# Optimization experiments

Hardware: AMD Instinct MI355X
Metric: run time of the kernel (lower is better)

## Reference

```python
import jax, jax.numpy as jnp
import numpy as np
from jax import lax

B, S, E, SD = 8, 4096, 1024, 8


def setup_inputs() -> dict:
    key = jax.random.key(0)
    ks = jax.random.split(key, 4)
    x = jax.random.normal(ks[0], (B, S, E), dtype=jnp.float32)
    W_in = jax.random.normal(ks[1], (E, E + SD), dtype=jnp.float32) / np.sqrt(E)
    b_in = jnp.zeros((E + SD,), dtype=jnp.float32)
    W_g = jax.random.normal(ks[2], (E + SD, SD), dtype=jnp.float32) / np.sqrt(E + SD)
    b_g = jnp.zeros((SD,), dtype=jnp.float32)
    W_out = jax.random.normal(ks[3], (E + SD, E), dtype=jnp.float32) / np.sqrt(E + SD)
    b_out = jnp.zeros((E,), dtype=jnp.float32)
    return {"x": x, "W_in": W_in, "b_in": b_in, "W_g": W_g, "b_g": b_g,
            "W_out": W_out, "b_out": b_out}


def reference(x, W_in, b_in, W_g, b_g, W_out, b_out):
    embed_dim = W_in.shape[0]
    # State-independent projections batched over the whole sequence.
    combined = jnp.einsum('bse,ec->bsc', x, W_in) + b_in            # [B,S,E+SD]
    embed = combined[..., :embed_dim]                                # [B,S,E]
    state_in = combined[..., embed_dim:]                             # [B,S,SD]
    gate = jax.nn.sigmoid(jnp.einsum('bsc,cd->bsd', combined, W_g) + b_g)  # [B,S,SD]

    # Only the tiny gated state recurrence is sequential.
    def step(state, gs):
        g, si = gs
        new = g * state + (1.0 - g) * si
        return new, new

    state0 = jnp.zeros((x.shape[0], state_in.shape[-1]), dtype=x.dtype)
    g_t = jnp.moveaxis(gate, 1, 0)        # [S,B,SD]
    si_t = jnp.moveaxis(state_in, 1, 0)   # [S,B,SD]
    final_state, states = lax.scan(step, state0, (g_t, si_t))
    states = jnp.moveaxis(states, 0, 1)   # [B,S,SD]

    out = jnp.einsum('bsc,cd->bsd', jnp.concatenate([embed, states], axis=-1), W_out) + b_out
    return out, final_state
```

## Files before the change

### kernel.cpp

```cpp
#include <hip/hip_runtime.h>

typedef unsigned short ushort_t;
typedef __attribute__((ext_vector_type(8))) short short8;
typedef __attribute__((ext_vector_type(4))) float floatx4;

#define B_ 8
#define S_ 4096
#define E_ 1024
#define SD_ 8
#define M_TOTAL (B_ * S_)
#define NC 1032
#define NCH 256
#define CHS (S_ / NCH)

__device__ __forceinline__ ushort_t f2bf(float f) {
    union { float f; unsigned u; } v; v.f = f;
    unsigned u = v.u;
    unsigned r = (u + 0x7fffu + ((u >> 16) & 1u)) >> 16;
    return (ushort_t)r;
}
__device__ __forceinline__ float bf2f(ushort_t h) {
    union { unsigned u; float f; } v; v.u = ((unsigned)h) << 16;
    return v.f;
}

__device__ __forceinline__ void stage16(ushort_t* lds_base_uniform, const ushort_t* g) {
    __builtin_amdgcn_global_load_lds(
        (const __attribute__((address_space(1))) void*)g,
        (__attribute__((address_space(3))) void*)lds_base_uniform, 16, 0, 0);
}


__global__ void wcomb_kernel(const float* __restrict__ W_in, const float* __restrict__ Wg,
                             float* __restrict__ Wc) {
    const int k = blockIdx.x;
    const int lane = threadIdx.x;
    float acc[8] = {0.f,0.f,0.f,0.f,0.f,0.f,0.f,0.f};
    for (int c = lane; c < NC; c += 64) {
        float w = W_in[(size_t)k * NC + c];
#pragma unroll
        for (int d = 0; d < 8; d++) acc[d] += w * Wg[(size_t)c * 8 + d];
    }
#pragma unroll
    for (int d = 0; d < 8; d++) {
#pragma unroll
        for (int off = 32; off >= 1; off >>= 1) acc[d] += __shfl_xor(acc[d], off);
    }
    if (lane == 0) {
#pragma unroll
        for (int d = 0; d < 8; d++) Wc[k * 8 + d] = acc[d];
    }
}

__global__ void prep_winb(const float* __restrict__ W, ushort_t* __restrict__ O) {
    int i = blockIdx.x * 256 + threadIdx.x;
    int k = i >> 8, j0 = (i & 255) * 4;
    float4 v = *(const float4*)(W + (size_t)k * NC + j0);
    ushort4 o;
    o.x = f2bf(v.x); o.y = f2bf(v.y); o.z = f2bf(v.z); o.w = f2bf(v.w);
    *(ushort4*)(O + (size_t)k * E_ + j0) = o;
}

__global__ void prep_wouts(const float* __restrict__ W, ushort_t* __restrict__ O) {
    int idx = blockIdx.x * 256 + threadIdx.x;
    int n = idx >> 10, j = idx & 1023;
    O[idx] = f2bf(W[(size_t)j * E_ + n]);
}

__global__ void prep_small(const float* __restrict__ W_in, const float* __restrict__ Wc,
                           const float* __restrict__ W_out, const float* __restrict__ b_in,
                           const float* __restrict__ Wg, const float* __restrict__ bg,
                           ushort_t* __restrict__ BT16, ushort_t* __restrict__ WoutT2,
                           float* __restrict__ bias16) {
    int idx = blockIdx.x * 256 + threadIdx.x;
    if (idx < 32768) {
        int n = idx >> 10, k = idx & 1023;
        float v;
        if (n < 8)        v = W_in[(size_t)k * NC + 1024 + n];
        else if (n < 16)  v = Wc[k * 8 + (n - 8)];
        else              v = 0.f;
        BT16[idx] = f2bf(v);
    } else {
        int i2 = idx - 32768;
        int n = i2 >> 5, k2 = i2 & 31;
        float v = (k2 < 8) ? W_out[(size_t)(1024 + k2) * E_ + n] : 0.f;
        WoutT2[i2] = f2bf(v);
    }
    if (idx < 32) {
        float s;
        if (idx < 8) s = b_in[1024 + idx];
        else if (idx < 16) {
            int d = idx - 8;
            s = bg[d];
            for (int j = 0; j < NC; j++) s += b_in[j] * Wg[(size_t)j * 8 + d];
        } else s = 0.f;
        bias16[idx] = s;
    }
}

__global__ void bias2_kernel(const float* __restrict__ b_in, const float* __restrict__ W_out,
                             const float* __restrict__ b_out, float* __restrict__ bias2) {
    int n = blockIdx.x * 64 + threadIdx.x;
    float acc = b_out[n];
    for (int j = 0; j < E_; j++) acc += b_in[j] * W_out[(size_t)j * E_ + n];
    bias2[n] = acc;
}

template <bool OUT_BF16, bool EXTRA>
__global__ __launch_bounds__(256, 2) void gemm_bt(
    const ushort_t* __restrict__ A, const ushort_t* __restrict__ BT,
    const ushort_t* __restrict__ A2, const ushort_t* __restrict__ BT2,
    void* __restrict__ Cout, const float* __restrict__ bias,
    int K, int lda, int ldb, int lda2, int ldb2, int ldc)
{
    __shared__ __align__(16) ushort_t sA[128 * 32];
    __shared__ __align__(16) ushort_t sB[128 * 32];
    const int tid = threadIdx.x;
    const int wave = tid >> 6;
    const int lane = tid & 63;

    const int gx = gridDim.x;
    int flat = blockIdx.y * gx + blockIdx.x;
    const int band_size = 8 * gx;
    int band = flat / band_size;
    int r = flat - band * band_size;
    const int m0 = (band * 8 + (r & 7)) * 128;
    const int n0 = (r >> 3) * 128;

    const int wm = wave >> 1, wn = wave & 1;
    const int fr = lane & 15, fq = lane >> 4;
    const int sr = lane >> 2;
    const int sc = (lane & 3) * 8;

    floatx4 acc[4][4];
#pragma unroll
    for (int i = 0; i < 4; i++)
#pragma unroll
        for (int j = 0; j < 4; j++) acc[i][j] = (floatx4)0.f;

    const ushort_t* gA = A + (size_t)(m0 + wave * 32 + sr) * lda + sc;
    const ushort_t* gB = BT + (size_t)(n0 + wave * 32 + sr) * ldb + sc;

    for (int k0 = 0; k0 < K; k0 += 32) {
        __syncthreads();
        stage16(&sA[(wave * 32 + 0) * 32], gA + k0);
        stage16(&sA[(wave * 32 + 16) * 32], gA + (size_t)16 * lda + k0);
        stage16(&sB[(wave * 32 + 0) * 32], gB + k0);
        stage16(&sB[(wave * 32 + 16) * 32], gB + (size_t)16 * ldb + k0);
        __syncthreads();

        short8 a[4], b[4];
#pragma unroll
        for (int i = 0; i < 4; i++)
            a[i] = *(const short8*)&sA[(wm * 64 + i * 16 + fr) * 32 + fq * 8];
#pragma unroll
        for (int j = 0; j < 4; j++)
            b[j] = *(const short8*)&sB[(wn * 64 + j * 16 + fr) * 32 + fq * 8];
#pragma unroll
        for (int i = 0; i < 4; i++)
#pragma unroll
            for (int j = 0; j < 4; j++)
                acc[i][j] = __builtin_amdgcn_mfma_f32_16x16x32_bf16(a[i], b[j], acc[i][j], 0, 0, 0);
    }

    if constexpr (EXTRA) {
        const ushort_t* gA2 = A2 + (size_t)(m0 + wave * 32 + sr) * lda2 + sc;
        const ushort_t* gB2 = BT2 + (size_t)(n0 + wave * 32 + sr) * ldb2 + sc;
        __syncthreads();
        stage16(&sA[(wave * 32 + 0) * 32], gA2);
        stage16(&sA[(wave * 32 + 16) * 32], gA2 + (size_t)16 * lda2);
        stage16(&sB[(wave * 32 + 0) * 32], gB2);
        stage16(&sB[(wave * 32 + 16) * 32], gB2 + (size_t)16 * ldb2);
        __syncthreads();

        short8 a[4], b[4];
#pragma unroll
        for (int i = 0; i < 4; i++)
            a[i] = *(const short8*)&sA[(wm * 64 + i * 16 + fr) * 32 + fq * 8];
#pragma unroll
        for (int j = 0; j < 4; j++)
            b[j] = *(const short8*)&sB[(wn * 64 + j * 16 + fr) * 32 + fq * 8];
#pragma unroll
        for (int i = 0; i < 4; i++)
#pragma unroll
            for (int j = 0; j < 4; j++)
                acc[i][j] = __builtin_amdgcn_mfma_f32_16x16x32_bf16(a[i], b[j], acc[i][j], 0, 0, 0);
    }

#pragma unroll
    for (int i = 0; i < 4; i++) {
        int row = m0 + wm * 64 + i * 16 + fq * 4;
#pragma unroll
        for (int j = 0; j < 4; j++) {
            int col = n0 + wn * 64 + j * 16 + fr;
            float bv = bias ? bias[col] : 0.f;
#pragma unroll
            for (int r2 = 0; r2 < 4; r2++) {
                float v = acc[i][j][r2] + bv;
                if (OUT_BF16)
                    ((ushort_t*)Cout)[(size_t)(row + r2) * ldc + col] = f2bf(v);
                else
                    ((float*)Cout)[(size_t)(row + r2) * ldc + col] = v;
            }
        }
    }
}

__global__ __launch_bounds__(256) void skinny16_cvt(
    const float* __restrict__ X,
    const ushort_t* __restrict__ BT,
    const float* __restrict__ bias,
    ushort_t* __restrict__ xb,
    ushort_t* __restrict__ C)
{
    const int tid = threadIdx.x, wave = tid >> 6, lane = tid & 63;
    const int m0 = blockIdx.x * 64 + wave * 16;
    const int fr = lane & 15, fq = lane >> 4;
    floatx4 acc0 = (floatx4)0.f;
    const float*    px  = X  + (size_t)(m0 + fr) * E_ + fq * 8;
    ushort_t*       pxb = xb + (size_t)(m0 + fr) * E_ + fq * 8;
    const ushort_t* pb0 = BT + (size_t)fr * E_ + fq * 8;
    for (int k0 = 0; k0 < E_; k0 += 32) {
        float4 v0 = *(const float4*)(px + k0);
        float4 v1 = *(const float4*)(px + k0 + 4);
        short8 a;
        a[0] = (short)f2bf(v0.x); a[1] = (short)f2bf(v0.y);
        a[2] = (short)f2bf(v0.z); a[3] = (short)f2bf(v0.w);
        a[4] = (short)f2bf(v1.x); a[5] = (short)f2bf(v1.y);
        a[6] = (short)f2bf(v1.z); a[7] = (short)f2bf(v1.w);
        *(short8*)(pxb + k0) = a;
        short8 b0 = *(const short8*)(pb0 + k0);
        acc0 = __builtin_amdgcn_mfma_f32_16x16x32_bf16(a, b0, acc0, 0, 0, 0);
    }
#pragma unroll
    for (int r = 0; r < 4; r++) {
        int row = m0 + fq * 4 + r;
        C[(size_t)row * 32 + fr]      = f2bf(acc0[r] + bias[fr]);
        C[(size_t)row * 32 + 16 + fr] = (ushort_t)0;
    }
}

__global__ void scan_chunks(const ushort_t* __restrict__ comb,
                            float* __restrict__ chA, float* __restrict__ chB)
{
    const int c = blockIdx.x, lane = threadIdx.x;
    const int b = lane >> 3, d = lane & 7;
    float A = 1.f, Bv = 0.f;
    const int s0 = c * CHS;
    for (int s = s0; s < s0 + CHS; s++) {
        size_t m = (size_t)b * S_ + s;
        float z = bf2f(comb[m * 32 + 8 + d]);
        float g = 1.f / (1.f + __expf(-z));
        float si = bf2f(comb[m * 32 + d]);
        Bv = g * Bv + (1.f - g) * si;
        A *= g;
    }
    chA[c * 64 + lane] = A;
    chB[c * 64 + lane] = Bv;
}

__global__ void scan_apply(ushort_t* __restrict__ comb,
                           const float* __restrict__ chA, const float* __restrict__ chB,
                           float* __restrict__ final_state)
{
    const int c = blockIdx.x, lane = threadIdx.x;
    const int b = lane >> 3, d = lane & 7;
    float state = 0.f;
    for (int j = 0; j < c; j++)
        state = chA[j * 64 + lane] * state + chB[j * 64 + lane];
    const int s0 = c * CHS;
    for (int s = s0; s < s0 + CHS; s++) {
        size_t m = (size_t)b * S_ + s;
        float z = bf2f(comb[m * 32 + 8 + d]);
        float g = 1.f / (1.f + __expf(-z));
        float si = bf2f(comb[m * 32 + d]);
        state = g * state + (1.f - g) * si;
        comb[m * 32 + d] = f2bf(state);
    }
    if (c == NCH - 1) final_state[lane] = state;
}

extern "C" void kernel_launch(void* const* d_in, const int* in_sizes, int n_in,
                              void* d_out, int out_size, void* d_ws, size_t ws_size,
                              hipStream_t stream)
{
    (void)in_sizes; (void)n_in; (void)out_size; (void)ws_size;
    const float* x     = (const float*)d_in[0];
    const float* W_in  = (const float*)d_in[1];
    const float* b_in  = (const float*)d_in[2];
    const float* W_g   = (const float*)d_in[3];
    const float* b_g   = (const float*)d_in[4];
    const float* W_out = (const float*)d_in[5];
    const float* b_out = (const float*)d_in[6];

    ushort_t* xb     = (ushort_t*)d_ws;
    ushort_t* comb16 = xb + (size_t)M_TOTAL * E_;
    ushort_t* WbigT  = comb16 + (size_t)M_TOTAL * 32;
    ushort_t* Winb   = WbigT + (size_t)E_ * E_;
    ushort_t* WoutTa = Winb + (size_t)E_ * E_;
    ushort_t* WoutT2 = WoutTa + (size_t)E_ * E_;
    ushort_t* BT16   = WoutT2 + (size_t)E_ * 32;
    float*    Wc     = (float*)(BT16 + (size_t)32 * E_);
    float*    bias16 = Wc + 1024 * 8;
    float*    bias2v = bias16 + 32;
    float*    chA    = bias2v + E_;
    float*    chB    = chA + NCH * 64;

    float* outp = (float*)d_out;
    float* fs = outp + (size_t)M_TOTAL * E_;

    wcomb_kernel<<<E_, 64, 0, stream>>>(W_in, W_g, Wc);
    prep_winb<<<1024, 256, 0, stream>>>(W_in, Winb);
    prep_wouts<<<(E_ * E_) / 256, 256, 0, stream>>>(W_out, WoutTa);
    prep_small<<<256, 256, 0, stream>>>(W_in, Wc, W_out, b_in, W_g, b_g, BT16, WoutT2, bias16);
    bias2_kernel<<<E_ / 64, 64, 0, stream>>>(b_in, W_out, b_out, bias2v);

    gemm_bt<true, false><<<dim3(E_ / 128, E_ / 128), 256, 0, stream>>>(
        WoutTa, Winb, nullptr, nullptr, WbigT, nullptr, E_, E_, E_, 0, 0, E_);

    skinny16_cvt<<<M_TOTAL / 64, 256, 0, stream>>>(x, BT16, bias16, xb, comb16);

    scan_chunks<<<NCH, 64, 0, stream>>>(comb16, chA, chB);
    scan_apply<<<NCH, 64, 0, stream>>>(comb16, chA, chB, fs);

    gemm_bt<false, true><<<dim3(E_ / 128, M_TOTAL / 128), 256, 0, stream>>>(
        xb, WbigT, comb16, WoutT2, outp, bias2v, E_, E_, E_, 32, 32, E_);
}
```

Baseline: 502.6 us.

## Split skinny GEMM K across waves and fuse chunked scan into one block-scan kernel

The skinny x·W16 projection now gives each wave a quarter of K for a 16-row tile and reduces the partial sums in shared memory, so the grid has four times as many blocks. The two-kernel chunked scan, which recombined chunk prefixes serially, is replaced by one kernel per (batch, state-dim) pair. Each block computes 256 sub-chunk summaries, does a Hillis-Steele prefix scan in LDS, then applies the result. This removes one launch and the serial prefix loop, at the cost of more syncs and strided 2-byte global accesses.

```diff
diff --git a/kernel.cpp b/kernel.cpp
--- a/kernel.cpp
+++ b/kernel.cpp
@@ -10,8 +10,6 @@
 #define SD_ 8
 #define M_TOTAL (B_ * S_)
 #define NC 1032
-#define NCH 256
-#define CHS (S_ / NCH)
 
 __device__ __forceinline__ ushort_t f2bf(float f) {
     union { float f; unsigned u; } v; v.f = f;
@@ -214,70 +212,84 @@
     ushort_t* __restrict__ C)
 {
     const int tid = threadIdx.x, wave = tid >> 6, lane = tid & 63;
-    const int m0 = blockIdx.x * 64 + wave * 16;
+    const int m0 = blockIdx.x * 16;
     const int fr = lane & 15, fq = lane >> 4;
-    floatx4 acc0 = (floatx4)0.f;
-    const float*    px  = X  + (size_t)(m0 + fr) * E_ + fq * 8;
-    ushort_t*       pxb = xb + (size_t)(m0 + fr) * E_ + fq * 8;
-    const ushort_t* pb0 = BT + (size_t)fr * E_ + fq * 8;
-    for (int k0 = 0; k0 < E_; k0 += 32) {
-        float4 v0 = *(const float4*)(px + k0);
-        float4 v1 = *(const float4*)(px + k0 + 4);
+    const int k0w = wave * 256;
+
+    floatx4 acc = (floatx4)0.f;
+    const float*    px  = X  + (size_t)(m0 + fr) * E_ + k0w + fq * 8;
+    ushort_t*       pxb = xb + (size_t)(m0 + fr) * E_ + k0w + fq * 8;
+    const ushort_t* pb  = BT + (size_t)fr * E_ + k0w + fq * 8;
+#pragma unroll
+    for (int kk = 0; kk < 256; kk += 32) {
+        float4 v0 = *(const float4*)(px + kk);
+        float4 v1 = *(const float4*)(px + kk + 4);
         short8 a;
         a[0] = (short)f2bf(v0.x); a[1] = (short)f2bf(v0.y);
         a[2] = (short)f2bf(v0.z); a[3] = (short)f2bf(v0.w);
         a[4] = (short)f2bf(v1.x); a[5] = (short)f2bf(v1.y);
         a[6] = (short)f2bf(v1.z); a[7] = (short)f2bf(v1.w);
-        *(short8*)(pxb + k0) = a;
-        short8 b0 = *(const short8*)(pb0 + k0);
-        acc0 = __builtin_amdgcn_mfma_f32_16x16x32_bf16(a, b0, acc0, 0, 0, 0);
-    }
-#pragma unroll
-    for (int r = 0; r < 4; r++) {
-        int row = m0 + fq * 4 + r;
-        C[(size_t)row * 32 + fr]      = f2bf(acc0[r] + bias[fr]);
-        C[(size_t)row * 32 + 16 + fr] = (ushort_t)0;
-    }
-}
-
-__global__ void scan_chunks(const ushort_t* __restrict__ comb,
-                            float* __restrict__ chA, float* __restrict__ chB)
+        *(short8*)(pxb + kk) = a;
+        short8 b0 = *(const short8*)(pb + kk);
+        acc = __builtin_amdgcn_mfma_f32_16x16x32_bf16(a, b0, acc, 0, 0, 0);
+    }
+
+    __shared__ float red[4][16][16];
+#pragma unroll
+    for (int r = 0; r < 4; r++) red[wave][fq * 4 + r][fr] = acc[r];
+    __syncthreads();
+    const int row = tid >> 4, col = tid & 15;
+    float v = red[0][row][col] + red[1][row][col] + red[2][row][col] + red[3][row][col]
+            + bias[col];
+    C[(size_t)(m0 + row) * 32 + col]      = f2bf(v);
+    C[(size_t)(m0 + row) * 32 + 16 + col] = (ushort_t)0;
+}
+
+__global__ __launch_bounds__(256) void scan_fused(
+    ushort_t* __restrict__ comb, float* __restrict__ final_state)
 {
-    const int c = blockIdx.x, lane = threadIdx.x;
-    const int b = lane >> 3, d = lane & 7;
+    const int b = blockIdx.x >> 3, d = blockIdx.x & 7;
+    const int t = threadIdx.x;
+    __shared__ float sA[256], sB[256];
+    const size_t base = (size_t)b * S_ * 32;
+    const int s0 = t * 16;
+
     float A = 1.f, Bv = 0.f;
-    const int s0 = c * CHS;
-    for (int s = s0; s < s0 + CHS; s++) {
-        size_t m = (size_t)b * S_ + s;
-        float z = bf2f(comb[m * 32 + 8 + d]);
+    for (int s = s0; s < s0 + 16; s++) {
+        size_t m = base + (size_t)s * 32;
+        float z = bf2f(comb[m + 8 + d]);
         float g = 1.f / (1.f + __expf(-z));
-        float si = bf2f(comb[m * 32 + d]);
+        float si = bf2f(comb[m + d]);
         Bv = g * Bv + (1.f - g) * si;
         A *= g;
     }
-    chA[c * 64 + lane] = A;
-    chB[c * 64 + lane] = Bv;
-}
-
-__global__ void scan_apply(ushort_t* __restrict__ comb,
-                           const float* __restrict__ chA, const float* __restrict__ chB,
-                           float* __restrict__ final_state)
-{
-    const int c = blockIdx.x, lane = threadIdx.x;
-    const int b = lane >> 3, d = lane & 7;
-    float state = 0.f;
-    for (int j = 0; j < c; j++)
-        state = chA[j * 64 + lane] * state + chB[j * 64 + lane];
-    const int s0 = c * CHS;
-    for (int s = s0; s < s0 + CHS; s++) {
-        size_t m = (size_t)b * S_ + s;
-        float z = bf2f(comb[m * 32 + 8 + d]);
+    sA[t] = A; sB[t] = Bv;
+    __syncthreads();
+
+    float rA = A, rB = Bv;
+    for (int off = 1; off < 256; off <<= 1) {
+        float a = 1.f, b_ = 0.f;
+        if (t >= off) { a = sA[t - off]; b_ = sB[t - off]; }
+        __syncthreads();
+        if (t >= off) {
+            float nA = a * rA;
+            float nB = rA * b_ + rB;
+            rA = nA; rB = nB;
+        }
+        sA[t] = rA; sB[t] = rB;
+        __syncthreads();
+    }
+
+    float state = (t == 0) ? 0.f : sB[t - 1];
+    for (int s = s0; s < s0 + 16; s++) {
+        size_t m = base + (size_t)s * 32;
+        float z = bf2f(comb[m + 8 + d]);
         float g = 1.f / (1.f + __expf(-z));
-        float si = bf2f(comb[m * 32 + d]);
+        float si = bf2f(comb[m + d]);
         state = g * state + (1.f - g) * si;
-        comb[m * 32 + d] = f2bf(state);
-    }
-    if (c == NCH - 1) final_state[lane] = state;
+        comb[m + d] = f2bf(state);
+    }
+    if (t == 255) final_state[b * 8 + d] = state;
 }
 
 extern "C" void kernel_launch(void* const* d_in, const int* in_sizes, int n_in,
@@ -303,8 +315,6 @@
     float*    Wc     = (float*)(BT16 + (size_t)32 * E_);
     float*    bias16 = Wc + 1024 * 8;
     float*    bias2v = bias16 + 32;
-    float*    chA    = bias2v + E_;
-    float*    chB    = chA + NCH * 64;
 
     float* outp = (float*)d_out;
     float* fs = outp + (size_t)M_TOTAL * E_;
@@ -318,10 +328,9 @@
     gemm_bt<true, false><<<dim3(E_ / 128, E_ / 128), 256, 0, stream>>>(
         WoutTa, Winb, nullptr, nullptr, WbigT, nullptr, E_, E_, E_, 0, 0, E_);
 
-    skinny16_cvt<<<M_TOTAL / 64, 256, 0, stream>>>(x, BT16, bias16, xb, comb16);
-
-    scan_chunks<<<NCH, 64, 0, stream>>>(comb16, chA, chB);
-    scan_apply<<<NCH, 64, 0, stream>>>(comb16, chA, chB, fs);
+    skinny16_cvt<<<M_TOTAL / 16, 256, 0, stream>>>(x, BT16, bias16, xb, comb16);
+
+    scan_fused<<<64, 256, 0, stream>>>(comb16, fs);
 
     gemm_bt<false, true><<<dim3(E_ / 128, M_TOTAL / 128), 256, 0, stream>>>(
         xb, WbigT, comb16, WoutT2, outp, bias2v, E_, E_, E_, 32, 32, E_);
```

Result: faster. 453.5 us (-9.8%).
